# Performance work log

Measured on AMD Instinct MI355X. Metric: run time of the kernel, lower is better.

## Reference

```python
import jax, jax.numpy as jnp
import numpy as np

K = 1024
D = 64
BETA = 0.25


def setup_inputs() -> dict:
    key = jax.random.key(0)
    k1, k2 = jax.random.split(key)
    latents = jax.random.normal(k1, (32, 64, 64, 64), dtype=jnp.float32)  # [B, C=D, H, W]
    # embedding init: uniform(-1/K, 1/K)
    embedding = jax.random.uniform(k2, (K, D), dtype=jnp.float32, minval=-1.0 / K, maxval=1.0 / K)
    return {"latents": latents, "embedding": embedding}


def reference(latents, embedding):
    # [B, D, H, W] -> [B, H, W, D]
    x = jnp.transpose(latents, (0, 2, 3, 1))
    shp = x.shape
    flat = x.reshape(-1, D)  # [N, D]

    dist = (jnp.sum(flat ** 2, axis=1, keepdims=True)
            + jnp.sum(embedding ** 2, axis=1)
            - 2.0 * flat @ embedding.T)  # [N, K]
    inds = jnp.argmin(dist, axis=1)  # [N]

    quantized = embedding[inds].reshape(shp)  # gather == one-hot @ embedding

    commitment_loss = jnp.mean((jax.lax.stop_gradient(quantized) - x) ** 2)
    embedding_loss = jnp.mean((quantized - jax.lax.stop_gradient(x)) ** 2)
    vq_loss = commitment_loss * BETA + embedding_loss

    # straight-through estimator
    quantized = x + jax.lax.stop_gradient(quantized - x)
    out = jnp.transpose(quantized, (0, 3, 1, 2))  # back to [B, D, H, W]
    return out, vq_loss
```

## Files before the change

kernel.cpp:

```cpp
#include <hip/hip_runtime.h>
#include <hip/hip_bf16.h>


#define HW 4096
#define OUTELEMS 8388608

typedef __attribute__((ext_vector_type(8))) short bf16x8;
typedef __attribute__((ext_vector_type(4))) float f32x4;
typedef __attribute__((ext_vector_type(4))) int i32x4;

static __device__ __forceinline__ short f2bf(float f) {
    union { __hip_bfloat16 h; short s; } u;
    u.h = __float2bfloat16(f);
    return u.s;
}
static __device__ __forceinline__ unsigned umin2(unsigned a, unsigned b) {
    return a < b ? a : b;
}


__global__ __launch_bounds__(256) void prep_kernel(const float* __restrict__ emb,
                                                   char* __restrict__ ws,
                                                   float* __restrict__ en1) {
    int code = blockIdx.x * 4 + (threadIdx.x >> 6);
    int d = threadIdx.x & 63;
    float v = emb[code * 64 + d];
    int ct = code >> 4, n = code & 15;
    int kk = d & 31;
    int l  = (kk >> 3) * 16 + n;
    int off = (d < 32 ? 0 : 65536) + ct * 1024 + l * 16 + (kk & 7) * 2;
    *(short*)(ws + off) = f2bf(-2.0f * v);
    float s = v * v;
#pragma unroll
    for (int o = 32; o > 0; o >>= 1) s += __shfl_xor(s, o, 64);
    if (d == 0) en1[code] = 1.0f + s;
}

__global__ __launch_bounds__(1024, 4) void vq_kernel(
        const float* __restrict__ lat, const float* __restrict__ wsrc,
        float* __restrict__ out, float* __restrict__ loss) {
    extern __shared__ __align__(16) char sbuf[];
    const int tid  = threadIdx.x;
    const int wave = tid >> 6;
    const int lane = tid & 63;
    const int n    = lane & 15;
    const int quad = lane >> 4;

    const int g0 = blockIdx.x * 512;
    const int b  = g0 >> 12;
    const int mb = g0 & 4095;
    const float* latb = lat + (size_t)b * 262144;

    {
        const f32x4* src = (const f32x4*)wsrc;
        f32x4* dst = (f32x4*)sbuf;
#pragma unroll
        for (int r = 0; r < 8; ++r)
            dst[r * 1024 + tid] = src[r * 1024 + tid];
        if (tid < 256)
            dst[8192 + tid] = src[8192 + tid];
    }

    bf16x8 bfr[2][2];
    float xnorm[2];
#pragma unroll
    for (int s = 0; s < 2; ++s) {
        const float* xp = latb + (mb + wave * 32 + s * 16 + n);
        float xs = 0.0f; bf16x8 f0, f1;
#pragma unroll
        for (int j = 0; j < 8; ++j) {
            float x0 = xp[(quad * 8 + j) * HW];
            float x1 = xp[(32 + quad * 8 + j) * HW];
            xs += x0 * x0 + x1 * x1;
            f0[j] = f2bf(x0); f1[j] = f2bf(x1);
        }
        bfr[s][0] = f0; bfr[s][1] = f1; xnorm[s] = xs;
    }
    __syncthreads();

    const char* A0 = sbuf;
    const char* A1 = sbuf + 65536;
    const f32x4* enl = (const f32x4*)(sbuf + 131072);
    const int lo = lane * 16;
    unsigned emin[2] = {0xFFFFFFFFu, 0xFFFFFFFFu};

    bf16x8 a0 = *(const bf16x8*)(A0 + lo);
    bf16x8 a1 = *(const bf16x8*)(A1 + lo);
    f32x4 en4 = enl[quad];

#pragma unroll 4
    for (int ct = 0; ct < 64; ++ct) {
        const int nx = (ct + 1) & 63;
        bf16x8 na0 = *(const bf16x8*)(A0 + nx * 1024 + lo);
        bf16x8 na1 = *(const bf16x8*)(A1 + nx * 1024 + lo);
        f32x4 nen = enl[nx * 4 + quad];

        f32x4 acc0 = __builtin_amdgcn_mfma_f32_16x16x32_bf16(a0, bfr[0][0], en4, 0, 0, 0);
        f32x4 acc1 = __builtin_amdgcn_mfma_f32_16x16x32_bf16(a0, bfr[1][0], en4, 0, 0, 0);
        acc0 = __builtin_amdgcn_mfma_f32_16x16x32_bf16(a1, bfr[0][1], acc0, 0, 0, 0);
        acc1 = __builtin_amdgcn_mfma_f32_16x16x32_bf16(a1, bfr[1][1], acc1, 0, 0, 0);

        const unsigned cb = ct * 16 + quad * 4;
        unsigned e0 = (__float_as_uint(acc0[0]) & 0xFFFFFC00u) | (cb + 0);
        unsigned e1 = (__float_as_uint(acc0[1]) & 0xFFFFFC00u) | (cb + 1);
        unsigned e2 = (__float_as_uint(acc0[2]) & 0xFFFFFC00u) | (cb + 2);
        unsigned e3 = (__float_as_uint(acc0[3]) & 0xFFFFFC00u) | (cb + 3);
        emin[0] = umin2(umin2(umin2(e0, e1), umin2(e2, e3)), emin[0]);
        unsigned f0 = (__float_as_uint(acc1[0]) & 0xFFFFFC00u) | (cb + 0);
        unsigned f1 = (__float_as_uint(acc1[1]) & 0xFFFFFC00u) | (cb + 1);
        unsigned f2 = (__float_as_uint(acc1[2]) & 0xFFFFFC00u) | (cb + 2);
        unsigned f3 = (__float_as_uint(acc1[3]) & 0xFFFFFC00u) | (cb + 3);
        emin[1] = umin2(umin2(umin2(f0, f1), umin2(f2, f3)), emin[1]);

        a0 = na0; a1 = na1; en4 = nen;
    }

#pragma unroll
    for (int off = 16; off <= 32; off <<= 1) {
#pragma unroll
        for (int s = 0; s < 2; ++s) {
            unsigned eo = (unsigned)__shfl_xor((int)emin[s], off, 64);
            float xo = __shfl_xor(xnorm[s], off, 64);
            emin[s] = eo < emin[s] ? eo : emin[s];
            xnorm[s] += xo;
        }
    }

    int* codes = (int*)(sbuf + 135168);
    if (quad == 0) {
        codes[wave * 32 + n]      = (int)(emin[0] & 1023u);
        codes[wave * 32 + 16 + n] = (int)(emin[1] & 1023u);
    }

    float contrib = 0.0f;
#pragma unroll
    for (int s = 0; s < 2; ++s)
        contrib += __uint_as_float(emin[s] & 0xFFFFFC00u) - 1.0f + xnorm[s];
#pragma unroll
    for (int off = 32; off > 0; off >>= 1) contrib += __shfl_xor(contrib, off, 64);
    float* wsum = (float*)(sbuf + 137216);
    if (lane == 0) wsum[wave] = contrib;
    __syncthreads();
    if (tid == 0) {
        float t = 0.0f;
#pragma unroll
        for (int w = 0; w < 16; ++w) t += wsum[w];
        atomicAdd(loss, t * (1.25f / (8388608.0f * 4.0f)));
    }

    float* outb = out + (size_t)b * 262144 + mb;
#pragma unroll 4
    for (int i = 0; i < 8; ++i) {
        int id = i * 1024 + tid;
        int d  = __builtin_amdgcn_readfirstlane(id >> 7);
        int mq = (id & 127) * 4;
        i32x4 c4 = *(const i32x4*)(codes + mq);
        const char* base = sbuf + (d < 32 ? 0 : 65536)
                         + ((d & 31) >> 3) * 256 + (d & 7) * 2;
        unsigned u0 = *(const unsigned short*)(base + (c4.x >> 4) * 1024 + (c4.x & 15) * 16);
        unsigned u1 = *(const unsigned short*)(base + (c4.y >> 4) * 1024 + (c4.y & 15) * 16);
        unsigned u2 = *(const unsigned short*)(base + (c4.z >> 4) * 1024 + (c4.z & 15) * 16);
        unsigned u3 = *(const unsigned short*)(base + (c4.w >> 4) * 1024 + (c4.w & 15) * 16);
        f32x4 v;
        v[0] = __uint_as_float(u0 << 16) * -0.5f;
        v[1] = __uint_as_float(u1 << 16) * -0.5f;
        v[2] = __uint_as_float(u2 << 16) * -0.5f;
        v[3] = __uint_as_float(u3 << 16) * -0.5f;
        *(f32x4*)(outb + d * HW + mq) = v;
    }
}

extern "C" void kernel_launch(void* const* d_in, const int* in_sizes, int n_in,
                              void* d_out, int out_size, void* d_ws, size_t ws_size,
                              hipStream_t stream) {
    const float* latents   = (const float*)d_in[0];
    const float* embedding = (const float*)d_in[1];
    float* out  = (float*)d_out;
    float* loss = out + OUTELEMS;

    char* ws = (char*)d_ws;
    float* en1 = (float*)(ws + 131072);

    hipFuncSetAttribute((const void*)vq_kernel,
                        hipFuncAttributeMaxDynamicSharedMemorySize, 137280);

    prep_kernel<<<256, 256, 0, stream>>>(embedding, ws, en1);
    vq_kernel<<<256, 1024, 137280, stream>>>(latents, (const float*)ws, out, loss);
}
```

Baseline: 107.1 us.

## Swap GEMM roles: keep codebook slice in registers, stream latents from LDS

Each wave now holds a fixed 64-code slice of the codebook in registers and iterates over all 512 latent vectors of the block, which are staged in LDS as bf16. Before, each wave held its 32 latents in registers and streamed the full codebook from LDS. Per-wave partial argmins are combined through LDS atomicMin slots. The codebook is copied into LDS only after the distance phase, for the gather step. This cuts the up-front 128KB LDS fill before compute and reorganises the packed layout, but it adds LDS atomics and an extra barrier per block.

```diff
diff --git a/kernel.cpp b/kernel.cpp
--- a/kernel.cpp
+++ b/kernel.cpp
@@ -25,10 +25,9 @@
     int code = blockIdx.x * 4 + (threadIdx.x >> 6);
     int d = threadIdx.x & 63;
     float v = emb[code * 64 + d];
-    int ct = code >> 4, n = code & 15;
     int kk = d & 31;
-    int l  = (kk >> 3) * 16 + n;
-    int off = (d < 32 ? 0 : 65536) + ct * 1024 + l * 16 + (kk & 7) * 2;
+    int off = (code >> 4) * 2048 + (d >> 5) * 1024 + (kk >> 3) * 256
+            + (code & 15) * 16 + (kk & 7) * 2;
     *(short*)(ws + off) = f2bf(-2.0f * v);
     float s = v * v;
 #pragma unroll
@@ -37,8 +36,9 @@
 }
 
 __global__ __launch_bounds__(1024, 4) void vq_kernel(
-        const float* __restrict__ lat, const float* __restrict__ wsrc,
-        float* __restrict__ out, float* __restrict__ loss) {
+        const float* __restrict__ lat, const char* __restrict__ wst,
+        const float* __restrict__ en1, float* __restrict__ out,
+        float* __restrict__ loss) {
     extern __shared__ __align__(16) char sbuf[];
     const int tid  = threadIdx.x;
     const int wave = tid >> 6;
@@ -51,102 +51,110 @@
     const int mb = g0 & 4095;
     const float* latb = lat + (size_t)b * 262144;
 
+    unsigned* slots = (unsigned*)(sbuf + 131072);
+    float*    xns   = (float*)(sbuf + 139264);
+    int*      codes = (int*)(sbuf + 141312);
+
+    slots[tid] = 0xFFFFFFFFu;
+    slots[1024 + tid] = 0xFFFFFFFFu;
+
+    bf16x8 A[4][2];
+    f32x4  enp[4];
     {
-        const f32x4* src = (const f32x4*)wsrc;
+        const char* at = wst + wave * 8192;
+#pragma unroll
+        for (int p = 0; p < 4; ++p) {
+            A[p][0] = *(const bf16x8*)(at + p * 2048 + lane * 16);
+            A[p][1] = *(const bf16x8*)(at + p * 2048 + 1024 + lane * 16);
+            enp[p]  = *(const f32x4*)(en1 + wave * 64 + p * 16 + quad * 4);
+        }
+    }
+
+    {
+        bf16x8 bfr[2][2];
+        float xnorm[2];
+#pragma unroll
+        for (int s = 0; s < 2; ++s) {
+            const float* xp = latb + (mb + wave * 32 + s * 16 + n);
+            float xs = 0.0f; bf16x8 f0, f1;
+#pragma unroll
+            for (int j = 0; j < 8; ++j) {
+                float x0 = xp[(quad * 8 + j) * HW];
+                float x1 = xp[(32 + quad * 8 + j) * HW];
+                xs += x0 * x0 + x1 * x1;
+                f0[j] = f2bf(x0); f1[j] = f2bf(x1);
+            }
+            bfr[s][0] = f0; bfr[s][1] = f1; xnorm[s] = xs;
+        }
+#pragma unroll
+        for (int off = 16; off <= 32; off <<= 1) {
+            xnorm[0] += __shfl_xor(xnorm[0], off, 64);
+            xnorm[1] += __shfl_xor(xnorm[1], off, 64);
+        }
+        if (quad == 0) {
+            xns[wave * 32 + n]      = xnorm[0];
+            xns[wave * 32 + 16 + n] = xnorm[1];
+        }
+#pragma unroll
+        for (int s = 0; s < 2; ++s) {
+            *(bf16x8*)(sbuf + ((wave * 2 + s) * 2 + 0) * 1024 + lane * 16) = bfr[s][0];
+            *(bf16x8*)(sbuf + ((wave * 2 + s) * 2 + 1) * 1024 + lane * 16) = bfr[s][1];
+        }
+    }
+    __syncthreads();
+
+    const int lo = lane * 16;
+    bf16x8 b0 = *(const bf16x8*)(sbuf + lo);
+    bf16x8 b1 = *(const bf16x8*)(sbuf + 1024 + lo);
+
+#pragma unroll 2
+    for (int pt = 0; pt < 32; ++pt) {
+        const int nx = (pt + 1) & 31;
+        bf16x8 nb0 = *(const bf16x8*)(sbuf + nx * 2048 + lo);
+        bf16x8 nb1 = *(const bf16x8*)(sbuf + nx * 2048 + 1024 + lo);
+
+        f32x4 acc[4];
+#pragma unroll
+        for (int p = 0; p < 4; ++p)
+            acc[p] = __builtin_amdgcn_mfma_f32_16x16x32_bf16(A[p][0], b0, enp[p], 0, 0, 0);
+#pragma unroll
+        for (int p = 0; p < 4; ++p)
+            acc[p] = __builtin_amdgcn_mfma_f32_16x16x32_bf16(A[p][1], b1, acc[p], 0, 0, 0);
+
+        unsigned enc = 0xFFFFFFFFu;
+#pragma unroll
+        for (int p = 0; p < 4; ++p) {
+            const unsigned cb = wave * 64 + p * 16 + quad * 4;
+            unsigned e0 = (__float_as_uint(acc[p][0]) & 0xFFFFFC00u) | (cb + 0);
+            unsigned e1 = (__float_as_uint(acc[p][1]) & 0xFFFFFC00u) | (cb + 1);
+            unsigned e2 = (__float_as_uint(acc[p][2]) & 0xFFFFFC00u) | (cb + 2);
+            unsigned e3 = (__float_as_uint(acc[p][3]) & 0xFFFFFC00u) | (cb + 3);
+            enc = umin2(enc, umin2(umin2(e0, e1), umin2(e2, e3)));
+        }
+        atomicMin(&slots[(pt * 16 + n) * 4 + quad], enc);
+
+        b0 = nb0; b1 = nb1;
+    }
+    __syncthreads();
+
+    {
+        const f32x4* src = (const f32x4*)wst;
         f32x4* dst = (f32x4*)sbuf;
 #pragma unroll
         for (int r = 0; r < 8; ++r)
             dst[r * 1024 + tid] = src[r * 1024 + tid];
-        if (tid < 256)
-            dst[8192 + tid] = src[8192 + tid];
     }
 
-    bf16x8 bfr[2][2];
-    float xnorm[2];
+    if (tid < 512) {
+        unsigned e = umin2(umin2(slots[4 * tid], slots[4 * tid + 1]),
+                           umin2(slots[4 * tid + 2], slots[4 * tid + 3]));
+        codes[tid] = (int)(e & 1023u);
+        float sc = __uint_as_float(e & 0xFFFFFC00u) - 1.0f + xns[tid];
 #pragma unroll
-    for (int s = 0; s < 2; ++s) {
-        const float* xp = latb + (mb + wave * 32 + s * 16 + n);
-        float xs = 0.0f; bf16x8 f0, f1;
-#pragma unroll
-        for (int j = 0; j < 8; ++j) {
-            float x0 = xp[(quad * 8 + j) * HW];
-            float x1 = xp[(32 + quad * 8 + j) * HW];
-            xs += x0 * x0 + x1 * x1;
-            f0[j] = f2bf(x0); f1[j] = f2bf(x1);
-        }
-        bfr[s][0] = f0; bfr[s][1] = f1; xnorm[s] = xs;
+        for (int off = 32; off > 0; off >>= 1) sc += __shfl_xor(sc, off, 64);
+        if (lane == 0) atomicAdd(loss, sc * (1.25f / 8388608.0f));
     }
     __syncthreads();
-
-    const char* A0 = sbuf;
-    const char* A1 = sbuf + 65536;
-    const f32x4* enl = (const f32x4*)(sbuf + 131072);
-    const int lo = lane * 16;
-    unsigned emin[2] = {0xFFFFFFFFu, 0xFFFFFFFFu};
-
-    bf16x8 a0 = *(const bf16x8*)(A0 + lo);
-    bf16x8 a1 = *(const bf16x8*)(A1 + lo);
-    f32x4 en4 = enl[quad];
-
-#pragma unroll 4
-    for (int ct = 0; ct < 64; ++ct) {
-        const int nx = (ct + 1) & 63;
-        bf16x8 na0 = *(const bf16x8*)(A0 + nx * 1024 + lo);
-        bf16x8 na1 = *(const bf16x8*)(A1 + nx * 1024 + lo);
-        f32x4 nen = enl[nx * 4 + quad];
-
-        f32x4 acc0 = __builtin_amdgcn_mfma_f32_16x16x32_bf16(a0, bfr[0][0], en4, 0, 0, 0);
-        f32x4 acc1 = __builtin_amdgcn_mfma_f32_16x16x32_bf16(a0, bfr[1][0], en4, 0, 0, 0);
-        acc0 = __builtin_amdgcn_mfma_f32_16x16x32_bf16(a1, bfr[0][1], acc0, 0, 0, 0);
-        acc1 = __builtin_amdgcn_mfma_f32_16x16x32_bf16(a1, bfr[1][1], acc1, 0, 0, 0);
-
-        const unsigned cb = ct * 16 + quad * 4;
-        unsigned e0 = (__float_as_uint(acc0[0]) & 0xFFFFFC00u) | (cb + 0);
-        unsigned e1 = (__float_as_uint(acc0[1]) & 0xFFFFFC00u) | (cb + 1);
-        unsigned e2 = (__float_as_uint(acc0[2]) & 0xFFFFFC00u) | (cb + 2);
-        unsigned e3 = (__float_as_uint(acc0[3]) & 0xFFFFFC00u) | (cb + 3);
-        emin[0] = umin2(umin2(umin2(e0, e1), umin2(e2, e3)), emin[0]);
-        unsigned f0 = (__float_as_uint(acc1[0]) & 0xFFFFFC00u) | (cb + 0);
-        unsigned f1 = (__float_as_uint(acc1[1]) & 0xFFFFFC00u) | (cb + 1);
-        unsigned f2 = (__float_as_uint(acc1[2]) & 0xFFFFFC00u) | (cb + 2);
-        unsigned f3 = (__float_as_uint(acc1[3]) & 0xFFFFFC00u) | (cb + 3);
-        emin[1] = umin2(umin2(umin2(f0, f1), umin2(f2, f3)), emin[1]);
-
-        a0 = na0; a1 = na1; en4 = nen;
-    }
-
-#pragma unroll
-    for (int off = 16; off <= 32; off <<= 1) {
-#pragma unroll
-        for (int s = 0; s < 2; ++s) {
-            unsigned eo = (unsigned)__shfl_xor((int)emin[s], off, 64);
-            float xo = __shfl_xor(xnorm[s], off, 64);
-            emin[s] = eo < emin[s] ? eo : emin[s];
-            xnorm[s] += xo;
-        }
-    }
-
-    int* codes = (int*)(sbuf + 135168);
-    if (quad == 0) {
-        codes[wave * 32 + n]      = (int)(emin[0] & 1023u);
-        codes[wave * 32 + 16 + n] = (int)(emin[1] & 1023u);
-    }
-
-    float contrib = 0.0f;
-#pragma unroll
-    for (int s = 0; s < 2; ++s)
-        contrib += __uint_as_float(emin[s] & 0xFFFFFC00u) - 1.0f + xnorm[s];
-#pragma unroll
-    for (int off = 32; off > 0; off >>= 1) contrib += __shfl_xor(contrib, off, 64);
-    float* wsum = (float*)(sbuf + 137216);
-    if (lane == 0) wsum[wave] = contrib;
-    __syncthreads();
-    if (tid == 0) {
-        float t = 0.0f;
-#pragma unroll
-        for (int w = 0; w < 16; ++w) t += wsum[w];
-        atomicAdd(loss, t * (1.25f / (8388608.0f * 4.0f)));
-    }
 
     float* outb = out + (size_t)b * 262144 + mb;
 #pragma unroll 4
@@ -155,12 +163,11 @@
         int d  = __builtin_amdgcn_readfirstlane(id >> 7);
         int mq = (id & 127) * 4;
         i32x4 c4 = *(const i32x4*)(codes + mq);
-        const char* base = sbuf + (d < 32 ? 0 : 65536)
-                         + ((d & 31) >> 3) * 256 + (d & 7) * 2;
-        unsigned u0 = *(const unsigned short*)(base + (c4.x >> 4) * 1024 + (c4.x & 15) * 16);
-        unsigned u1 = *(const unsigned short*)(base + (c4.y >> 4) * 1024 + (c4.y & 15) * 16);
-        unsigned u2 = *(const unsigned short*)(base + (c4.z >> 4) * 1024 + (c4.z & 15) * 16);
-        unsigned u3 = *(const unsigned short*)(base + (c4.w >> 4) * 1024 + (c4.w & 15) * 16);
+        const char* base = sbuf + (d >> 5) * 1024 + ((d & 31) >> 3) * 256 + (d & 7) * 2;
+        unsigned u0 = *(const unsigned short*)(base + (c4.x >> 4) * 2048 + (c4.x & 15) * 16);
+        unsigned u1 = *(const unsigned short*)(base + (c4.y >> 4) * 2048 + (c4.y & 15) * 16);
+        unsigned u2 = *(const unsigned short*)(base + (c4.z >> 4) * 2048 + (c4.z & 15) * 16);
+        unsigned u3 = *(const unsigned short*)(base + (c4.w >> 4) * 2048 + (c4.w & 15) * 16);
         f32x4 v;
         v[0] = __uint_as_float(u0 << 16) * -0.5f;
         v[1] = __uint_as_float(u1 << 16) * -0.5f;
@@ -182,8 +189,8 @@
     float* en1 = (float*)(ws + 131072);
 
     hipFuncSetAttribute((const void*)vq_kernel,
-                        hipFuncAttributeMaxDynamicSharedMemorySize, 137280);
+                        hipFuncAttributeMaxDynamicSharedMemorySize, 143424);
 
     prep_kernel<<<256, 256, 0, stream>>>(embedding, ws, en1);
-    vq_kernel<<<256, 1024, 137280, stream>>>(latents, (const float*)ws, out, loss);
+    vq_kernel<<<256, 1024, 143424, stream>>>(latents, ws, en1, out, loss);
 }
```

New measurement: 127.2 us. 1.19x slower.
